# Kernel tuning notes

Hardware: AMD Instinct MI355X
Metric: run time of the kernel (lower is better)

The kernel has to match this reference:

```python
import jax, jax.numpy as jnp
import numpy as np
from jax import lax

IMG = 1024.0
STRIDES = (8.0, 16.0, 32.0)
REG_MAX = 7
TOP_K = 100          # top_k_n
IOU_THR = 0.5        # hard-coded in the original combined_non_max_suppression call
BOX_SCORE = 0.3
NMS_PRE = 1000       # hard-coded in get_bboxes
B, C = 8, 80
HWS = ((128, 128), (64, 64), (32, 32))


def setup_inputs() -> dict:
    key = jax.random.key(0)
    ks = jax.random.split(key, 6)
    inp = {}
    for i, (h, w) in enumerate(HWS):
        inp[f'cls{i}'] = jax.random.normal(ks[2 * i], (B, h, w, C), dtype=jnp.float32)
        inp[f'bp{i}'] = jax.random.normal(ks[2 * i + 1], (B, h, w, 4 * (REG_MAX + 1)), dtype=jnp.float32)
    inp['origin_shapes'] = jnp.tile(jnp.array([[1080.0, 1920.0]], dtype=jnp.float32), (B, 1))
    return inp


def _decode_level(cls, bp, stride):
    # cls: [H,W,C]; bp: [H,W,4*(REG_MAX+1)] for one image/one level
    H, W, Cc = cls.shape
    y = (jnp.arange(H, dtype=jnp.float32) + 0.5) * stride
    x = (jnp.arange(W, dtype=jnp.float32) + 0.5) * stride
    yy, xx = jnp.meshgrid(y, x, indexing='ij')
    pts = jnp.stack([yy.ravel(), xx.ravel()], axis=-1)            # [N,2] = (y, x)
    scores = jax.nn.sigmoid(cls.reshape(-1, Cc))                  # [N,C]
    # DFL: softmax over reg_max+1 bins, expectation = distance
    proj = jnp.arange(REG_MAX + 1, dtype=jnp.float32)
    dist = (jax.nn.softmax(bp.reshape(-1, REG_MAX + 1), axis=-1) @ proj)
    dist = dist.reshape(-1, 4) * stride                           # [N,4] (l,t,r,b)
    if H * W > NMS_PRE:  # static per level
        top_idx = lax.top_k(scores.max(axis=-1), NMS_PRE)[1]
        pts, dist, scores = pts[top_idx], dist[top_idx], scores[top_idx]
    y1 = jnp.clip(pts[:, 0] - dist[:, 0], 0.0, IMG)
    x1 = jnp.clip(pts[:, 1] - dist[:, 1], 0.0, IMG)
    y2 = jnp.clip(pts[:, 0] + dist[:, 2], 0.0, IMG)
    x2 = jnp.clip(pts[:, 1] + dist[:, 3], 0.0, IMG)
    # original flips (y1,x1)->(x1,y1) and (y2,x2)->(x2,y2)
    boxes = jnp.stack([x1, y1, x2, y2], axis=-1)
    return boxes, scores


def _iou_one_vs_all(box, boxes):
    # box: [4], boxes: [N,4] in (x1,y1,x2,y2)
    xx1 = jnp.maximum(box[0], boxes[:, 0])
    yy1 = jnp.maximum(box[1], boxes[:, 1])
    xx2 = jnp.minimum(box[2], boxes[:, 2])
    yy2 = jnp.minimum(box[3], boxes[:, 3])
    inter = jnp.maximum(xx2 - xx1, 0.0) * jnp.maximum(yy2 - yy1, 0.0)
    a0 = jnp.maximum(box[2] - box[0], 0.0) * jnp.maximum(box[3] - box[1], 0.0)
    a1 = jnp.maximum(boxes[:, 2] - boxes[:, 0], 0.0) * jnp.maximum(boxes[:, 3] - boxes[:, 1], 0.0)
    return inter / jnp.maximum(a0 + a1 - inter, 1e-9)


def _nms_one_class(boxes, scores):
    # greedy NMS: pick argmax, suppress IoU > thr; fixed TOP_K iterations
    def step(sc, _):
        i = jnp.argmax(sc)
        s = sc[i]
        b = boxes[i]
        iou = _iou_one_vs_all(b, boxes)
        sc = jnp.where(iou > IOU_THR, -jnp.inf, sc)  # also kills i (iou=1)
        return sc, (b, s)
    _, (sel_b, sel_s) = lax.scan(step, scores, None, length=TOP_K)
    return sel_b, sel_s  # [K,4], [K]  (invalid slots have score=-inf)


def _forward(cls0, cls1, cls2, bp0, bp1, bp2, origin_shapes):
    decode = jax.vmap(_decode_level, in_axes=(0, 0, None))
    bxs, scs = [], []
    for c, bp, s in ((cls0, bp0, STRIDES[0]), (cls1, bp1, STRIDES[1]), (cls2, bp2, STRIDES[2])):
        b_l, s_l = decode(c, bp, s)
        bxs.append(b_l)
        scs.append(s_l)
    boxes = jnp.concatenate(bxs, axis=1)   # [B,N,4]
    scores = jnp.concatenate(scs, axis=1)  # [B,N,C]
    # combined NMS: per-class greedy NMS then global top-K (class-shared boxes)
    nms_bc = jax.vmap(jax.vmap(_nms_one_class, in_axes=(None, 1)), in_axes=(0, 0))
    sel_b, sel_s = nms_bc(boxes, scores)   # [B,C,K,4], [B,C,K]
    Bn = sel_s.shape[0]
    cls_ids = jnp.broadcast_to(jnp.arange(C, dtype=jnp.float32)[:, None], (C, TOP_K)).reshape(-1)
    flat_s = sel_s.reshape(Bn, -1)
    flat_b = sel_b.reshape(Bn, -1, 4)
    top_s, top_i = lax.top_k(flat_s, TOP_K)                         # [B,K]
    top_b = jnp.take_along_axis(flat_b, top_i[..., None], axis=1)   # [B,K,4]
    top_c = cls_ids[top_i]                                          # [B,K]
    valid = jnp.isfinite(top_s)
    nms_s = jnp.where(valid, top_s, 0.0)
    nms_b = jnp.where(valid[..., None], top_b, 0.0)
    nms_c = jnp.where(valid, top_c, 0.0)
    out = jnp.concatenate([nms_b, nms_s[..., None], nms_c[..., None]], axis=-1)  # [B,K,6]
    # original boolean-mask+ragged-reshape replaced by zeroing rows below box_score
    keep = nms_s > BOX_SCORE
    return jnp.where(keep[..., None], out, 0.0)


def reference(cls0, cls1, cls2, bp0, bp1, bp2, origin_shapes):
    return _forward(cls0, cls1, cls2, bp0, bp1, bp2, origin_shapes)
```

## Files before the change

### kernel.cpp

```cpp
#include <hip/hip_runtime.h>

#define BATCH 8
#define NCLS 80
#define APIX 21504
#define AL0 16384
#define AL1 20480
#define NSEL 3000
#define TOPK 100
#define NBINS 32768
#define BNDCAP 4096

__device__ __forceinline__ unsigned f2s(float f){
  unsigned u = __float_as_uint(f);
  return (u & 0x80000000u) ? ~u : (u | 0x80000000u);
}
__device__ __forceinline__ float s2f(unsigned u){
  return (u & 0x80000000u) ? __uint_as_float(u ^ 0x80000000u) : __uint_as_float(~u);
}
__device__ __forceinline__ float sigd(float x){
  return (float)(1.0 / (1.0 + exp(-(double)x)));
}
__device__ __forceinline__ float expd(float x){
  return (float)exp((double)x);
}

__global__ __launch_bounds__(256) void k_decode(
    const float* __restrict__ cls0, const float* __restrict__ cls1, const float* __restrict__ cls2,
    const float* __restrict__ bp0,  const float* __restrict__ bp1,  const float* __restrict__ bp2,
    unsigned* __restrict__ keys, float4* __restrict__ boxes, unsigned* __restrict__ hist){
  int gid = blockIdx.x*256 + threadIdx.x;
  if (gid >= BATCH*APIX) return;
  int b = gid / APIX, a = gid - b*APIX;
  const float *cls, *bp; int loc, W; float stride; int l;
  if (a < AL0){ l=0; loc=a;      W=128; stride=8.f;  cls=cls0 + (size_t)b*16384*80; bp=bp0 + (size_t)b*16384*32; }
  else if (a < AL1){ l=1; loc=a-AL0; W=64; stride=16.f; cls=cls1 + (size_t)b*4096*80; bp=bp1 + (size_t)b*4096*32; }
  else { l=2; loc=a-AL1; W=32; stride=32.f; cls=cls2 + (size_t)b*1024*80; bp=bp2 + (size_t)b*1024*32; }
  const float4* c4 = (const float4*)(cls + (size_t)loc*80);
  float m = -3.4e38f;
  #pragma unroll
  for (int i=0;i<20;i++){ float4 v = c4[i]; m = fmaxf(m, fmaxf(fmaxf(v.x,v.y), fmaxf(v.z,v.w))); }
  unsigned key = f2s(m);
  keys[gid] = key;
  atomicAdd(&hist[((b*3+l)<<15) + (key>>17)], 1u);

  const float4* p4 = (const float4*)(bp + (size_t)loc*32);
  float d[4];
  #pragma unroll
  for (int g=0; g<4; g++){
    float4 lo = p4[2*g], hi = p4[2*g+1];
    float mm = fmaxf(fmaxf(fmaxf(lo.x,lo.y),fmaxf(lo.z,lo.w)), fmaxf(fmaxf(hi.x,hi.y),fmaxf(hi.z,hi.w)));
    float e0=expd(lo.x-mm), e1=expd(lo.y-mm), e2=expd(lo.z-mm), e3=expd(lo.w-mm);
    float e4=expd(hi.x-mm), e5=expd(hi.y-mm), e6=expd(hi.z-mm), e7=expd(hi.w-mm);
    float s = e0+e1+e2+e3+e4+e5+e6+e7;
    float dot = (e1/s) + 2.f*(e2/s) + 3.f*(e3/s) + 4.f*(e4/s) + 5.f*(e5/s) + 6.f*(e6/s) + 7.f*(e7/s);
    d[g] = dot * stride;
  }
  float py = ((float)(loc / W) + 0.5f) * stride;
  float px = ((float)(loc % W) + 0.5f) * stride;
  float y1v = fminf(fmaxf(py - d[0], 0.f), 1024.f);
  float x1v = fminf(fmaxf(px - d[1], 0.f), 1024.f);
  float y2v = fminf(fmaxf(py + d[2], 0.f), 1024.f);
  float x2v = fminf(fmaxf(px + d[3], 0.f), 1024.f);
  boxes[gid] = make_float4(x1v, y1v, x2v, y2v);
}

__global__ __launch_bounds__(256) void k_thresh(const unsigned* __restrict__ hist,
                                                unsigned* __restrict__ thr){
  int bl = blockIdx.x;
  const unsigned* h = hist + ((size_t)bl << 15);
  __shared__ unsigned part[256];
  int t = threadIdx.x;
  unsigned sum = 0; int base = t*128;
  for (int i=0;i<128;i++) sum += h[base+i];
  part[t] = sum;
  __syncthreads();
  for (int off=1; off<256; off<<=1){
    unsigned v = part[t];
    unsigned add = (t+off < 256) ? part[t+off] : 0u;
    __syncthreads();
    part[t] = v + add;
    __syncthreads();
  }
  unsigned sfx = part[t];
  unsigned nxt = (t==255) ? 0u : part[t+1];
  if (sfx >= 1000u && nxt < 1000u){
    unsigned c = nxt;
    for (int u=127; u>=0; u--){
      unsigned hv = h[base+u];
      c += hv;
      if (c >= 1000u){
        thr[bl*4+0] = (unsigned)(base+u);
        thr[bl*4+1] = c - hv;
        thr[bl*4+2] = 1000u - (c - hv);
        break;
      }
    }
  }
}

__global__ __launch_bounds__(256) void k_select(const unsigned* __restrict__ keys,
    const unsigned* __restrict__ thr, unsigned* __restrict__ sel_cnt,
    unsigned* __restrict__ sel_idx, unsigned long long* __restrict__ bnd,
    unsigned* __restrict__ bnd_cnt){
  int gid = blockIdx.x*256 + threadIdx.x;
  int b = gid / APIX, a = gid - b*APIX;
  int l = (a < AL0) ? 0 : (a < AL1 ? 1 : 2);
  unsigned key = keys[gid];
  int bl = b*3 + l;
  unsigned T = thr[bl*4];
  unsigned bin = key >> 17;
  unsigned lane = threadIdx.x & 63;
  unsigned long long lt = (lane == 0) ? 0ull : (~0ull >> (64u - lane));
  bool is_sel = (bin > T), is_bnd = (bin == T);
  unsigned long long msel = __ballot(is_sel);
  unsigned long long mbnd = __ballot(is_bnd);
  unsigned sbase = 0, bbase = 0;
  if (lane == 0){
    if (msel) sbase = atomicAdd(&sel_cnt[bl], (unsigned)__popcll(msel));
    if (mbnd) bbase = atomicAdd(&bnd_cnt[bl], (unsigned)__popcll(mbnd));
  }
  sbase = __shfl(sbase, 0, 64);
  bbase = __shfl(bbase, 0, 64);
  if (is_sel){
    sel_idx[b*NSEL + l*1000 + sbase + (unsigned)__popcll(msel & lt)] = (unsigned)a;
  }
  if (is_bnd){
    unsigned q = bbase + (unsigned)__popcll(mbnd & lt);
    if (q < BNDCAP) bnd[(size_t)bl*BNDCAP + q] = ((unsigned long long)key << 32) | (0xFFFFFFFFu - (unsigned)a);
  }
}

__global__ __launch_bounds__(256) void k_bnd(const unsigned long long* __restrict__ bnd,
    const unsigned* __restrict__ bnd_cnt, const unsigned* __restrict__ thr,
    unsigned* __restrict__ sel_cnt, unsigned* __restrict__ sel_idx){
  int bl = blockIdx.x; int b = bl/3, l = bl%3;
  __shared__ unsigned long long sb[BNDCAP];
  unsigned Q = bnd_cnt[bl]; if (Q > (unsigned)BNDCAP) Q = BNDCAP;
  unsigned r = thr[bl*4 + 2];
  for (unsigned i=threadIdx.x; i<Q; i+=256) sb[i] = bnd[(size_t)bl*BNDCAP + i];
  __syncthreads();
  for (unsigned i=threadIdx.x; i<Q; i+=256){
    unsigned long long me = sb[i];
    unsigned rank = 0;
    for (unsigned j=0; j<Q; j++) rank += (sb[j] > me) ? 1u : 0u;
    if (rank < r){
      unsigned p = atomicAdd(&sel_cnt[bl], 1u);
      sel_idx[b*NSEL + l*1000 + p] = 0xFFFFFFFFu - (unsigned)(me & 0xFFFFFFFFull);
    }
  }
}

__global__ __launch_bounds__(512) void k_sortsel(const unsigned* __restrict__ keys,
                                                 unsigned* __restrict__ sel_idx){
  int bl = blockIdx.x; int b = bl/3, l = bl%3;
  __shared__ unsigned long long s[1024];
  unsigned* base = sel_idx + b*NSEL + l*1000;
  int t = threadIdx.x;
  for (int i=t; i<1024; i+=512){
    unsigned long long v = 0ull;
    if (i < 1000){
      unsigned a = base[i];
      v = ((unsigned long long)keys[(size_t)b*APIX + a] << 32) | (0xFFFFFFFFu - a);
    }
    s[i] = v;
  }
  __syncthreads();
  for (int k=2; k<=1024; k<<=1){
    for (int j=k>>1; j>0; j>>=1){
      for (int i=t; i<1024; i+=512){
        int ixj = i ^ j;
        if (ixj > i){
          bool up = ((i & k) == 0);
          unsigned long long x = s[i], y = s[ixj];
          bool sw = up ? (x < y) : (x > y);
          if (sw){ s[i] = y; s[ixj] = x; }
        }
      }
      __syncthreads();
    }
  }
  for (int i=t; i<1000; i+=512) base[i] = 0xFFFFFFFFu - (unsigned)(s[i] & 0xFFFFFFFFull);
}

__global__ __launch_bounds__(256) void k_gather(
    const float* __restrict__ cls0, const float* __restrict__ cls1, const float* __restrict__ cls2,
    const unsigned* __restrict__ sel_idx, const float4* __restrict__ boxes_dec,
    float* __restrict__ scores_t, float4* __restrict__ sel_boxes){
  int b = blockIdx.x / 47, tile = blockIdx.x % 47;
  int slot_base = tile*64;
  __shared__ float tilebuf[64][84];
  __shared__ unsigned sanchor[64];
  int t = threadIdx.x, sl = t & 63, cg = t >> 6;
  int slot = slot_base + sl;
  bool valid = slot < NSEL;
  if (t < 64){
    int s2 = slot_base + t;
    sanchor[t] = (s2 < NSEL) ? sel_idx[b*NSEL + s2] : 0u;
  }
  __syncthreads();
  unsigned a = sanchor[sl];
  const float* crow;
  if (a < AL0)      crow = cls0 + ((size_t)b*16384 + a)*80;
  else if (a < AL1) crow = cls1 + ((size_t)b*4096 + (a-AL0))*80;
  else              crow = cls2 + ((size_t)b*1024 + (a-AL1))*80;
  const float4* c4 = (const float4*)crow + cg*5;
  float4 v0=c4[0], v1=c4[1], v2=c4[2], v3=c4[3], v4=c4[4];
  float4* drow = (float4*)&tilebuf[sl][cg*20];
  drow[0]=v0; drow[1]=v1; drow[2]=v2; drow[3]=v3; drow[4]=v4;
  __syncthreads();
  #pragma unroll
  for (int it=0; it<20; it++){
    int cc = it*4 + cg;
    if (valid) scores_t[((size_t)b*NCLS + cc)*NSEL + slot] = sigd(tilebuf[sl][cc]);
  }
  if (t < 64 && slot_base + t < NSEL){
    unsigned aa = sanchor[t];
    sel_boxes[b*NSEL + slot_base + t] = boxes_dec[(size_t)b*APIX + aa];
  }
}

__global__ __launch_bounds__(256) void k_mask(const float4* __restrict__ selb,
                                              unsigned* __restrict__ mask32){
  int b = blockIdx.x / 47, tile = blockIdx.x % 47;
  int row_base = tile*64;
  __shared__ float4 jb[NSEL];
  for (int i=threadIdx.x; i<NSEL; i+=256) jb[i] = selb[b*NSEL + i];
  __syncthreads();
  int t = threadIdx.x;
  int r0 = t & 15, w = (t>>4)&3, l0 = t>>6;
  float4 ib[4]; float ia[4]; int irow[4];
  #pragma unroll
  for (int ri=0; ri<4; ri++){
    int i = row_base + r0 + 16*ri; irow[ri] = i;
    float4 v = jb[(i < NSEL) ? i : 0]; ib[ri]=v;
    ia[ri] = fmaxf(v.z-v.x,0.f)*fmaxf(v.w-v.y,0.f);
  }
  unsigned acc[4][8];
  #pragma unroll
  for (int ri=0; ri<4; ri++)
    #pragma unroll
    for (int z=0; z<8; z++) acc[ri][z] = 0u;
  for (int k=0;k<12;k++){
    #pragma unroll
    for (int li=0; li<16; li++){
      int j = k*256 + w*64 + l0*16 + li;
      if (j >= NSEL) continue;
      float4 jv = jb[j];
      float ja = fmaxf(jv.z-jv.x,0.f)*fmaxf(jv.w-jv.y,0.f);
      #pragma unroll
      for (int ri=0; ri<4; ri++){
        float xx1 = fmaxf(ib[ri].x, jv.x), yy1 = fmaxf(ib[ri].y, jv.y);
        float xx2 = fminf(ib[ri].z, jv.z), yy2 = fminf(ib[ri].w, jv.w);
        float inter = fmaxf(xx2-xx1,0.f)*fmaxf(yy2-yy1,0.f);
        float denom = fmaxf(ia[ri] + ja - inter, 1e-9f);
        float iou = inter / denom;
        if (iou > 0.5f) acc[ri][li>>1] |= (1u << (k + 16*(li&1)));
      }
    }
  }
  #pragma unroll
  for (int ri=0; ri<4; ri++){
    int i = irow[ri];
    if (i < NSEL){
      unsigned* dst = mask32 + ((size_t)(b*NSEL + i))*128 + (w*32 + l0*8);
      ((uint4*)dst)[0] = make_uint4(acc[ri][0],acc[ri][1],acc[ri][2],acc[ri][3]);
      ((uint4*)dst)[1] = make_uint4(acc[ri][4],acc[ri][5],acc[ri][6],acc[ri][7]);
    }
  }
}

__global__ __launch_bounds__(256) void k_nms(const float* __restrict__ scores_t,
    const unsigned short* __restrict__ mask16,
    float* __restrict__ nms_s, unsigned* __restrict__ nms_slot){
  int c = blockIdx.x, b = blockIdx.y;
  const float* sc = scores_t + ((size_t)b*NCLS + c)*NSEL;
  int tid = threadIdx.x;
  unsigned long long key[12];
  #pragma unroll
  for (int k=0;k<12;k++){
    int slot = k*256 + tid;
    unsigned hi = 0x007FFFFFu;
    if (slot < NSEL) hi = f2s(sc[slot]);
    key[k] = ((unsigned long long)hi << 32) | (unsigned)(3071 - slot);
  }
  __shared__ unsigned long long wred[4];
  float* outS = nms_s + ((size_t)b*NCLS + c)*TOPK;
  unsigned* outI = nms_slot + ((size_t)b*NCLS + c)*TOPK;
  int lane = tid & 63, wid = tid >> 6;
  for (int it=0; it<TOPK; it++){
    unsigned long long m = key[0];
    #pragma unroll
    for (int k=1;k<12;k++) m = key[k] > m ? key[k] : m;
    #pragma unroll
    for (int off=32; off; off>>=1){
      unsigned long long o = __shfl_xor(m, off, 64);
      m = o > m ? o : m;
    }
    if (lane == 0) wred[wid] = m;
    __syncthreads();
    unsigned long long m0 = wred[0], m1 = wred[1], m2 = wred[2], m3 = wred[3];
    unsigned long long ma = m0 > m1 ? m0 : m1;
    unsigned long long mb = m2 > m3 ? m2 : m3;
    unsigned long long mm = ma > mb ? ma : mb;
    unsigned slot = 3071u - (unsigned)(mm & 0xFFFFFFFFull);
    if (tid == 0){ outS[it] = s2f((unsigned)(mm>>32)); outI[it] = slot; }
    unsigned short mv = mask16[((size_t)(b*NSEL + slot))*256 + tid];
    #pragma unroll
    for (int k=0;k<12;k++){
      if ((mv >> k) & 1) key[k] = (0x007FFFFFull << 32) | (key[k] & 0xFFFFFFFFull);
    }
    __syncthreads();
  }
}

__global__ __launch_bounds__(256) void k_out(const float* __restrict__ nms_s,
    const unsigned* __restrict__ nms_slot, const float4* __restrict__ selb,
    float* __restrict__ out){
  int b = blockIdx.x >> 5, chunk = blockIdx.x & 31;
  __shared__ float ls[8000];
  for (int i=threadIdx.x; i<8000; i+=256) ls[i] = nms_s[(size_t)b*8000 + i];
  __syncthreads();
  if (threadIdx.x >= 250) return;
  int e = chunk*250 + threadIdx.x;
  int c = e / 100, k = e - c*100;
  float s = ls[e];
  if (!(s > 0.3f)) return;
  int rank = k;
  for (int c2=0; c2<NCLS; c2++){
    if (c2 == c) continue;
    const float* L = ls + c2*100;
    int lo=0, hi=100;
    while (lo < hi){ int mid=(lo+hi)>>1; if (L[mid] > s) lo=mid+1; else hi=mid; }
    if (c2 < c){
      int lo2=lo, hi2=100;
      while (lo2 < hi2){ int mid=(lo2+hi2)>>1; if (L[mid] >= s) lo2=mid+1; else hi2=mid; }
      rank += lo2;
    } else rank += lo;
    if (rank >= 100) return;
  }
  unsigned slot = nms_slot[(size_t)b*8000 + e];
  float4 bx = selb[b*NSEL + slot];
  float* o = out + ((size_t)b*100 + rank)*6;
  o[0]=bx.x; o[1]=bx.y; o[2]=bx.z; o[3]=bx.w; o[4]=s; o[5]=(float)c;
}

extern "C" void kernel_launch(void* const* d_in, const int* in_sizes, int n_in,
                              void* d_out, int out_size, void* d_ws, size_t ws_size,
                              hipStream_t stream){
  const float* cls0 = (const float*)d_in[0];
  const float* bp0  = (const float*)d_in[1];
  const float* cls1 = (const float*)d_in[2];
  const float* bp1  = (const float*)d_in[3];
  const float* cls2 = (const float*)d_in[4];
  const float* bp2  = (const float*)d_in[5];
  float* out = (float*)d_out;

  char* ws = (char*)d_ws;
  size_t off = 0;
  float*    scores_t  = (float*)(ws + off);              off += 7680000;
  unsigned* mask32    = (unsigned*)(ws + off);           off += 12288000;
  float4*   boxes_dec = (float4*)(ws + off);             off += 2752512;
  unsigned* keys      = (unsigned*)(ws + off);           off += 688128;
  unsigned* sel_idx   = (unsigned*)(ws + off);           off += 96000;
  float4*   sel_boxes = (float4*)(ws + off);             off += 384000;
  float*    nms_s     = (float*)(ws + off);              off += 256000;
  unsigned* nms_slot  = (unsigned*)(ws + off);           off += 256000;
  unsigned long long* bnd = (unsigned long long*)(ws + off); off += 786432;
  unsigned* thr       = (unsigned*)(ws + off);           off += 512;
  size_t zoff = off;
  unsigned* hist      = (unsigned*)(ws + off);           off += 3145728;
  unsigned* sel_cnt   = (unsigned*)(ws + off);           off += 128;
  unsigned* bnd_cnt   = (unsigned*)(ws + off);           off += 128;

  hipMemsetAsync(ws + zoff, 0, 3145728 + 256, stream);
  hipMemsetAsync(d_out, 0, (size_t)out_size * sizeof(float), stream);

  k_decode<<<672, 256, 0, stream>>>(cls0, cls1, cls2, bp0, bp1, bp2, keys, boxes_dec, hist);
  k_thresh<<<24, 256, 0, stream>>>(hist, thr);
  k_select<<<672, 256, 0, stream>>>(keys, thr, sel_cnt, sel_idx, bnd, bnd_cnt);
  k_bnd<<<24, 256, 0, stream>>>(bnd, bnd_cnt, thr, sel_cnt, sel_idx);
  k_sortsel<<<24, 512, 0, stream>>>(keys, sel_idx);
  k_gather<<<376, 256, 0, stream>>>(cls0, cls1, cls2, sel_idx, boxes_dec, scores_t, sel_boxes);
  k_mask<<<376, 256, 0, stream>>>(sel_boxes, mask32);
  dim3 gnms(NCLS, BATCH);
  k_nms<<<gnms, 256, 0, stream>>>(scores_t, (const unsigned short*)mask32, nms_s, nms_slot);
  k_out<<<256, 256, 0, stream>>>(nms_s, nms_slot, sel_boxes, out);
}
```

Before: 528.0 us.

## Rework NMS into single-wavefront blocks with 64-bit masks and cached maxima

The NMS suppression mask is re-laid out as 64-bit words per lane: bit k of lane t marks column k*64+t. This lets each class NMS run in one 64-thread wavefront, with no shared-memory reductions or block barriers per iteration. Each lane caches its running maximum and rescans its 47 keys only when its current best is suppressed. The boundary rank kernel and selection sort are fused into one launch, and the threshold kernel uses 1024 threads. The cost is more registers per NMS thread (47 keys) and a divergent rescan path.

```diff
diff --git a/kernel.cpp b/kernel.cpp
--- a/kernel.cpp
+++ b/kernel.cpp
@@ -64,28 +64,29 @@
   boxes[gid] = make_float4(x1v, y1v, x2v, y2v);
 }
 
-__global__ __launch_bounds__(256) void k_thresh(const unsigned* __restrict__ hist,
-                                                unsigned* __restrict__ thr){
+__global__ __launch_bounds__(1024) void k_thresh(const unsigned* __restrict__ hist,
+                                                 unsigned* __restrict__ thr){
   int bl = blockIdx.x;
   const unsigned* h = hist + ((size_t)bl << 15);
-  __shared__ unsigned part[256];
+  __shared__ unsigned part[1024];
   int t = threadIdx.x;
-  unsigned sum = 0; int base = t*128;
-  for (int i=0;i<128;i++) sum += h[base+i];
+  unsigned sum = 0; int base = t*32;
+  #pragma unroll
+  for (int i=0;i<32;i++) sum += h[base+i];
   part[t] = sum;
   __syncthreads();
-  for (int off=1; off<256; off<<=1){
+  for (int off=1; off<1024; off<<=1){
     unsigned v = part[t];
-    unsigned add = (t+off < 256) ? part[t+off] : 0u;
+    unsigned add = (t+off < 1024) ? part[t+off] : 0u;
     __syncthreads();
     part[t] = v + add;
     __syncthreads();
   }
   unsigned sfx = part[t];
-  unsigned nxt = (t==255) ? 0u : part[t+1];
+  unsigned nxt = (t==1023) ? 0u : part[t+1];
   if (sfx >= 1000u && nxt < 1000u){
     unsigned c = nxt;
-    for (int u=127; u>=0; u--){
+    for (int u=31; u>=0; u--){
       unsigned hv = h[base+u];
       c += hv;
       if (c >= 1000u){
@@ -130,16 +131,18 @@
   }
 }
 
-__global__ __launch_bounds__(256) void k_bnd(const unsigned long long* __restrict__ bnd,
+__global__ __launch_bounds__(512) void k_bndsort(const unsigned long long* __restrict__ bnd,
     const unsigned* __restrict__ bnd_cnt, const unsigned* __restrict__ thr,
+    const unsigned* __restrict__ keys,
     unsigned* __restrict__ sel_cnt, unsigned* __restrict__ sel_idx){
   int bl = blockIdx.x; int b = bl/3, l = bl%3;
   __shared__ unsigned long long sb[BNDCAP];
   unsigned Q = bnd_cnt[bl]; if (Q > (unsigned)BNDCAP) Q = BNDCAP;
   unsigned r = thr[bl*4 + 2];
-  for (unsigned i=threadIdx.x; i<Q; i+=256) sb[i] = bnd[(size_t)bl*BNDCAP + i];
-  __syncthreads();
-  for (unsigned i=threadIdx.x; i<Q; i+=256){
+  int t = threadIdx.x;
+  for (unsigned i=t; i<Q; i+=512) sb[i] = bnd[(size_t)bl*BNDCAP + i];
+  __syncthreads();
+  for (unsigned i=t; i<Q; i+=512){
     unsigned long long me = sb[i];
     unsigned rank = 0;
     for (unsigned j=0; j<Q; j++) rank += (sb[j] > me) ? 1u : 0u;
@@ -148,21 +151,16 @@
       sel_idx[b*NSEL + l*1000 + p] = 0xFFFFFFFFu - (unsigned)(me & 0xFFFFFFFFull);
     }
   }
-}
-
-__global__ __launch_bounds__(512) void k_sortsel(const unsigned* __restrict__ keys,
-                                                 unsigned* __restrict__ sel_idx){
-  int bl = blockIdx.x; int b = bl/3, l = bl%3;
-  __shared__ unsigned long long s[1024];
+  __threadfence_block();
+  __syncthreads();
   unsigned* base = sel_idx + b*NSEL + l*1000;
-  int t = threadIdx.x;
   for (int i=t; i<1024; i+=512){
     unsigned long long v = 0ull;
     if (i < 1000){
       unsigned a = base[i];
       v = ((unsigned long long)keys[(size_t)b*APIX + a] << 32) | (0xFFFFFFFFu - a);
     }
-    s[i] = v;
+    sb[i] = v;
   }
   __syncthreads();
   for (int k=2; k<=1024; k<<=1){
@@ -171,15 +169,15 @@
         int ixj = i ^ j;
         if (ixj > i){
           bool up = ((i & k) == 0);
-          unsigned long long x = s[i], y = s[ixj];
+          unsigned long long x = sb[i], y = sb[ixj];
           bool sw = up ? (x < y) : (x > y);
-          if (sw){ s[i] = y; s[ixj] = x; }
+          if (sw){ sb[i] = y; sb[ixj] = x; }
         }
       }
       __syncthreads();
     }
   }
-  for (int i=t; i<1000; i+=512) base[i] = 0xFFFFFFFFu - (unsigned)(s[i] & 0xFFFFFFFFull);
+  for (int i=t; i<1000; i+=512) base[i] = 0xFFFFFFFFu - (unsigned)(sb[i] & 0xFFFFFFFFull);
 }
 
 __global__ __launch_bounds__(256) void k_gather(
@@ -220,96 +218,92 @@
 }
 
 __global__ __launch_bounds__(256) void k_mask(const float4* __restrict__ selb,
-                                              unsigned* __restrict__ mask32){
+                                              unsigned long long* __restrict__ mask64){
   int b = blockIdx.x / 47, tile = blockIdx.x % 47;
   int row_base = tile*64;
   __shared__ float4 jb[NSEL];
   for (int i=threadIdx.x; i<NSEL; i+=256) jb[i] = selb[b*NSEL + i];
   __syncthreads();
-  int t = threadIdx.x;
-  int r0 = t & 15, w = (t>>4)&3, l0 = t>>6;
-  float4 ib[4]; float ia[4]; int irow[4];
-  #pragma unroll
-  for (int ri=0; ri<4; ri++){
-    int i = row_base + r0 + 16*ri; irow[ri] = i;
-    float4 v = jb[(i < NSEL) ? i : 0]; ib[ri]=v;
-    ia[ri] = fmaxf(v.z-v.x,0.f)*fmaxf(v.w-v.y,0.f);
-  }
-  unsigned acc[4][8];
-  #pragma unroll
-  for (int ri=0; ri<4; ri++)
-    #pragma unroll
-    for (int z=0; z<8; z++) acc[ri][z] = 0u;
-  for (int k=0;k<12;k++){
-    #pragma unroll
-    for (int li=0; li<16; li++){
-      int j = k*256 + w*64 + l0*16 + li;
-      if (j >= NSEL) continue;
+  int t = threadIdx.x & 63, w = threadIdx.x >> 6;
+  float4 ib[16]; float ia[16];
+  #pragma unroll
+  for (int r=0;r<16;r++){
+    int i = row_base + w*16 + r;
+    float4 v = jb[(i < NSEL) ? i : 0];
+    ib[r] = v;
+    ia[r] = fmaxf(v.z-v.x,0.f)*fmaxf(v.w-v.y,0.f);
+  }
+  unsigned long long acc[16];
+  #pragma unroll
+  for (int r=0;r<16;r++) acc[r] = 0ull;
+  for (int k=0;k<47;k++){
+    int j = k*64 + t;
+    if (j < NSEL){
       float4 jv = jb[j];
       float ja = fmaxf(jv.z-jv.x,0.f)*fmaxf(jv.w-jv.y,0.f);
       #pragma unroll
-      for (int ri=0; ri<4; ri++){
-        float xx1 = fmaxf(ib[ri].x, jv.x), yy1 = fmaxf(ib[ri].y, jv.y);
-        float xx2 = fminf(ib[ri].z, jv.z), yy2 = fminf(ib[ri].w, jv.w);
+      for (int r=0;r<16;r++){
+        float xx1 = fmaxf(ib[r].x, jv.x), yy1 = fmaxf(ib[r].y, jv.y);
+        float xx2 = fminf(ib[r].z, jv.z), yy2 = fminf(ib[r].w, jv.w);
         float inter = fmaxf(xx2-xx1,0.f)*fmaxf(yy2-yy1,0.f);
-        float denom = fmaxf(ia[ri] + ja - inter, 1e-9f);
-        float iou = inter / denom;
-        if (iou > 0.5f) acc[ri][li>>1] |= (1u << (k + 16*(li&1)));
+        float denom = fmaxf(ia[r] + ja - inter, 1e-9f);
+        if (2.f*inter >= denom){
+          float iou = inter / denom;
+          if (iou > 0.5f) acc[r] |= (1ull << k);
+        }
       }
     }
   }
   #pragma unroll
-  for (int ri=0; ri<4; ri++){
-    int i = irow[ri];
-    if (i < NSEL){
-      unsigned* dst = mask32 + ((size_t)(b*NSEL + i))*128 + (w*32 + l0*8);
-      ((uint4*)dst)[0] = make_uint4(acc[ri][0],acc[ri][1],acc[ri][2],acc[ri][3]);
-      ((uint4*)dst)[1] = make_uint4(acc[ri][4],acc[ri][5],acc[ri][6],acc[ri][7]);
-    }
-  }
-}
-
-__global__ __launch_bounds__(256) void k_nms(const float* __restrict__ scores_t,
-    const unsigned short* __restrict__ mask16,
+  for (int r=0;r<16;r++){
+    int i = row_base + w*16 + r;
+    if (i < NSEL) mask64[((size_t)(b*NSEL + i))*64 + t] = acc[r];
+  }
+}
+
+__global__ __launch_bounds__(64) void k_nms(const float* __restrict__ scores_t,
+    const unsigned long long* __restrict__ mask64,
     float* __restrict__ nms_s, unsigned* __restrict__ nms_slot){
-  int c = blockIdx.x, b = blockIdx.y;
+  int c = blockIdx.x >> 3, b = blockIdx.x & 7;
   const float* sc = scores_t + ((size_t)b*NCLS + c)*NSEL;
-  int tid = threadIdx.x;
-  unsigned long long key[12];
-  #pragma unroll
-  for (int k=0;k<12;k++){
-    int slot = k*256 + tid;
+  int t = threadIdx.x;
+  unsigned long long key[47];
+  #pragma unroll
+  for (int k=0;k<47;k++){
+    int slot = k*64 + t;
     unsigned hi = 0x007FFFFFu;
     if (slot < NSEL) hi = f2s(sc[slot]);
     key[k] = ((unsigned long long)hi << 32) | (unsigned)(3071 - slot);
   }
-  __shared__ unsigned long long wred[4];
+  unsigned long long tm = 0ull, killed = 0ull;
+  #pragma unroll
+  for (int k=0;k<47;k++) tm = key[k] > tm ? key[k] : tm;
   float* outS = nms_s + ((size_t)b*NCLS + c)*TOPK;
   unsigned* outI = nms_slot + ((size_t)b*NCLS + c)*TOPK;
-  int lane = tid & 63, wid = tid >> 6;
+  const unsigned long long* mrow = mask64 + (size_t)b*NSEL*64 + t;
+  #pragma unroll 1
   for (int it=0; it<TOPK; it++){
-    unsigned long long m = key[0];
-    #pragma unroll
-    for (int k=1;k<12;k++) m = key[k] > m ? key[k] : m;
+    unsigned long long m = tm;
     #pragma unroll
     for (int off=32; off; off>>=1){
       unsigned long long o = __shfl_xor(m, off, 64);
       m = o > m ? o : m;
     }
-    if (lane == 0) wred[wid] = m;
-    __syncthreads();
-    unsigned long long m0 = wred[0], m1 = wred[1], m2 = wred[2], m3 = wred[3];
-    unsigned long long ma = m0 > m1 ? m0 : m1;
-    unsigned long long mb = m2 > m3 ? m2 : m3;
-    unsigned long long mm = ma > mb ? ma : mb;
-    unsigned slot = 3071u - (unsigned)(mm & 0xFFFFFFFFull);
-    if (tid == 0){ outS[it] = s2f((unsigned)(mm>>32)); outI[it] = slot; }
-    unsigned short mv = mask16[((size_t)(b*NSEL + slot))*256 + tid];
-    #pragma unroll
-    for (int k=0;k<12;k++){
-      if ((mv >> k) & 1) key[k] = (0x007FFFFFull << 32) | (key[k] & 0xFFFFFFFFull);
-    }
-    __syncthreads();
+    unsigned slot = 3071u - (unsigned)(m & 0xFFFFFFFFull);
+    unsigned long long mv = mrow[(size_t)slot*64];
+    if (t == 0){ outS[it] = s2f((unsigned)(m>>32)); outI[it] = slot; }
+    killed |= mv;
+    unsigned myk = (3071u - (unsigned)(tm & 0xFFFFFFFFull)) >> 6;
+    if ((mv >> myk) & 1ull){
+      unsigned long long nm = 0ull;
+      #pragma unroll
+      for (int k=0;k<47;k++){
+        unsigned long long v = ((killed >> k) & 1ull)
+          ? ((0x007FFFFFull << 32) | (key[k] & 0xFFFFFFFFull)) : key[k];
+        nm = v > nm ? v : nm;
+      }
+      tm = nm;
+    }
   }
 }
 
@@ -358,7 +352,7 @@
   char* ws = (char*)d_ws;
   size_t off = 0;
   float*    scores_t  = (float*)(ws + off);              off += 7680000;
-  unsigned* mask32    = (unsigned*)(ws + off);           off += 12288000;
+  unsigned long long* mask64 = (unsigned long long*)(ws + off); off += 12288000;
   float4*   boxes_dec = (float4*)(ws + off);             off += 2752512;
   unsigned* keys      = (unsigned*)(ws + off);           off += 688128;
   unsigned* sel_idx   = (unsigned*)(ws + off);           off += 96000;
@@ -376,13 +370,11 @@
   hipMemsetAsync(d_out, 0, (size_t)out_size * sizeof(float), stream);
 
   k_decode<<<672, 256, 0, stream>>>(cls0, cls1, cls2, bp0, bp1, bp2, keys, boxes_dec, hist);
-  k_thresh<<<24, 256, 0, stream>>>(hist, thr);
+  k_thresh<<<24, 1024, 0, stream>>>(hist, thr);
   k_select<<<672, 256, 0, stream>>>(keys, thr, sel_cnt, sel_idx, bnd, bnd_cnt);
-  k_bnd<<<24, 256, 0, stream>>>(bnd, bnd_cnt, thr, sel_cnt, sel_idx);
-  k_sortsel<<<24, 512, 0, stream>>>(keys, sel_idx);
+  k_bndsort<<<24, 512, 0, stream>>>(bnd, bnd_cnt, thr, keys, sel_cnt, sel_idx);
   k_gather<<<376, 256, 0, stream>>>(cls0, cls1, cls2, sel_idx, boxes_dec, scores_t, sel_boxes);
-  k_mask<<<376, 256, 0, stream>>>(sel_boxes, mask32);
-  dim3 gnms(NCLS, BATCH);
-  k_nms<<<gnms, 256, 0, stream>>>(scores_t, (const unsigned short*)mask32, nms_s, nms_slot);
+  k_mask<<<376, 256, 0, stream>>>(sel_boxes, mask64);
+  k_nms<<<640, 64, 0, stream>>>(scores_t, mask64, nms_s, nms_slot);
   k_out<<<256, 256, 0, stream>>>(nms_s, nms_slot, sel_boxes, out);
 }
```

Result: slower. 554.1 us (+4.9%).
